# Performance work log

Measured on AMD Instinct MI355X. Metric: run time of the kernel, lower is better.

## Reference

```python
import jax, jax.numpy as jnp
import numpy as np

# Config (mirrors init_kwargs)
B, S = 1, 2048          # batch, seq_len
H = 2048                # hidden_size
NH, NKV = 16, 8         # attention heads, kv heads (GQA n_rep = 2)
HD = H // NH            # head_dim = 128
I = 5632                # intermediate_size
L = 2                   # num_hidden_layers
V = 32000               # vocab_size
WIN = 1024              # sliding_window
THETA = 10000.0
EPS = 1e-6


def setup_inputs() -> dict:
    key = jax.random.key(0)
    ks = jax.random.split(key, 12)
    s = 0.02
    return {
        "input_ids": jax.random.randint(ks[0], (B, S), 0, V, dtype=jnp.int32),
        "embed": jax.random.normal(ks[1], (V, H), jnp.float32) * s,
        "Wq": jax.random.normal(ks[2], (L, H, NH * HD), jnp.float32) * s,
        "Wk": jax.random.normal(ks[3], (L, H, NKV * HD), jnp.float32) * s,
        "Wv": jax.random.normal(ks[4], (L, H, NKV * HD), jnp.float32) * s,
        "Wo": jax.random.normal(ks[5], (L, NH * HD, H), jnp.float32) * s,
        "Wg": jax.random.normal(ks[6], (L, H, I), jnp.float32) * s,
        "Wu": jax.random.normal(ks[7], (L, H, I), jnp.float32) * s,
        "Wd": jax.random.normal(ks[8], (L, I, H), jnp.float32) * s,
        "ln1": jnp.ones((L, H), jnp.float32),
        "ln2": jnp.ones((L, H), jnp.float32),
        "norm_w": jnp.ones((H,), jnp.float32),
    }


def _rmsnorm(x, w, eps=EPS):
    return x * jax.lax.rsqrt(jnp.mean(x * x, axis=-1, keepdims=True) + eps) * w


def _rope_tables(seq_len, dim, theta):
    inv_freq = 1.0 / (theta ** (jnp.arange(0, dim, 2, dtype=jnp.float32) / dim))
    freqs = jnp.arange(seq_len, dtype=jnp.float32)[:, None] * inv_freq[None, :]  # [S, dim/2]
    emb = jnp.concatenate([freqs, freqs], axis=-1)  # [S, dim]
    return jnp.cos(emb), jnp.sin(emb)


def _rotate_half(x):
    half = x.shape[-1] // 2
    return jnp.concatenate([-x[..., half:], x[..., :half]], axis=-1)


def _sliding_window_causal_mask(seq_len, window, dtype):
    i = jnp.arange(seq_len)[:, None]
    j = jnp.arange(seq_len)[None, :]
    allowed = (j <= i) & (j >= i - window)  # band: causal + sliding window
    return jnp.where(allowed, 0.0, jnp.finfo(dtype).min).astype(dtype)[None, None]  # [1,1,S,S]


def _forward(input_ids, embed, Wq, Wk, Wv, Wo, Wg, Wu, Wd, ln1, ln2, norm_w):
    x = embed[input_ids]  # [B,S,H]
    cos, sin = _rope_tables(S, HD, THETA)          # [S,HD]
    cos = cos[None, :, None, :]                    # [1,S,1,HD]
    sin = sin[None, :, None, :]
    mask = _sliding_window_causal_mask(S, WIN, x.dtype)  # [1,1,S,S]
    scale = 1.0 / jnp.sqrt(jnp.float32(HD)).astype(x.dtype)
    n_rep = NH // NKV

    for l in range(L):
        # --- attention block ---
        h = _rmsnorm(x, ln1[l])
        q = (h @ Wq[l]).reshape(B, S, NH, HD)
        k = (h @ Wk[l]).reshape(B, S, NKV, HD)
        v = (h @ Wv[l]).reshape(B, S, NKV, HD)
        q = q * cos + _rotate_half(q) * sin
        k = k * cos + _rotate_half(k) * sin
        # repeat_kv (GQA)
        k = jnp.broadcast_to(k[:, :, :, None, :], (B, S, NKV, n_rep, HD)).reshape(B, S, NH, HD)
        v = jnp.broadcast_to(v[:, :, :, None, :], (B, S, NKV, n_rep, HD)).reshape(B, S, NH, HD)
        scores = jnp.einsum('bshn,bthn->bhst', q, k) * scale + mask  # [B,NH,S,S]
        attn = jax.nn.softmax(scores.astype(jnp.float32), axis=-1).astype(x.dtype)
        o = jnp.einsum('bhst,bthn->bshn', attn, v).reshape(B, S, NH * HD)
        x = x + o @ Wo[l]
        # --- MLP block (SwiGLU) ---
        h = _rmsnorm(x, ln2[l])
        x = x + (jax.nn.silu(h @ Wg[l]) * (h @ Wu[l])) @ Wd[l]

    return _rmsnorm(x, norm_w)


def reference(input_ids, embed, Wq, Wk, Wv, Wo, Wg, Wu, Wd, ln1, ln2, norm_w):
    return _forward(input_ids, embed, Wq, Wk, Wv, Wo, Wg, Wu, Wd, ln1, ln2, norm_w)
```

## Files before the change

kernel.cpp:

```cpp
#include <hip/hip_runtime.h>
#include <stdint.h>

using bf16x8 = __attribute__((ext_vector_type(8))) __bf16;
using f32x4  = __attribute__((ext_vector_type(4))) float;

#define DEVI __device__ __forceinline__

DEVI unsigned short f2b(float f) {
  unsigned int u = __builtin_bit_cast(unsigned int, f);
  u = (u + 0x7FFFu + ((u >> 16) & 1u)) >> 16;
  return (unsigned short)u;
}
DEVI float b2f(unsigned short h) {
  unsigned int u = ((unsigned int)h) << 16;
  return __builtin_bit_cast(float, u);
}
DEVI f32x4 mfma16(bf16x8 a, bf16x8 b, f32x4 c) {
  return __builtin_amdgcn_mfma_f32_16x16x32_bf16(a, b, c, 0, 0, 0);
}
#define GLD(gp, lp) __builtin_amdgcn_global_load_lds( \
    (__attribute__((address_space(1))) void*)(uintptr_t)(gp), \
    (__attribute__((address_space(3))) void*)(uintptr_t)(lp), 16, 0, 0)

static constexpr int S_LEN = 2048;
static constexpr int HDIM  = 2048;
static constexpr int NH    = 16;
static constexpr int NKV   = 8;
static constexpr int HD    = 128;
static constexpr int IFF   = 5632;
static constexpr int WIN   = 1024;

__global__ __launch_bounds__(64) void rope_tables_kernel(float* __restrict__ ct,
                                                         float* __restrict__ st) {
  int s = blockIdx.x, d = threadIdx.x;
  float inv = expf(-(float)d * (9.210340371976184f / 64.0f));
  float f = (float)s * inv;
  ct[s * 64 + d] = cosf(f);
  st[s * 64 + d] = sinf(f);
}

__global__ __launch_bounds__(256) void gather_kernel(const int* __restrict__ ids,
    const float* __restrict__ embed, float* __restrict__ x) {
  int s = blockIdx.x, t = threadIdx.x;
  const float4* src = (const float4*)(embed + (size_t)ids[s] * HDIM);
  float4* dst = (float4*)(x + (size_t)s * HDIM);
  dst[t]       = src[t];
  dst[t + 256] = src[t + 256];
}

DEVI void rms_finish(float4 v0, float4 v1, const float* __restrict__ w,
                     void* __restrict__ outp, int s, int t, int outf32) {
  float ss = v0.x*v0.x + v0.y*v0.y + v0.z*v0.z + v0.w*v0.w +
             v1.x*v1.x + v1.y*v1.y + v1.z*v1.z + v1.w*v1.w;
  #pragma unroll
  for (int off = 32; off >= 1; off >>= 1) ss += __shfl_xor(ss, off, 64);
  __shared__ float red[4];
  if ((t & 63) == 0) red[t >> 6] = ss;
  __syncthreads();
  ss = red[0] + red[1] + red[2] + red[3];
  float rr = rsqrtf(ss * (1.0f / 2048.0f) + 1e-6f);
  const float4* w4 = (const float4*)w;
  float4 w0 = w4[t], w1 = w4[t + 256];
  float o0x = v0.x*rr*w0.x, o0y = v0.y*rr*w0.y, o0z = v0.z*rr*w0.z, o0w = v0.w*rr*w0.w;
  float o1x = v1.x*rr*w1.x, o1y = v1.y*rr*w1.y, o1z = v1.z*rr*w1.z, o1w = v1.w*rr*w1.w;
  if (outf32) {
    float4* o4 = (float4*)outp + (size_t)s * 512;
    o4[t]       = make_float4(o0x, o0y, o0z, o0w);
    o4[t + 256] = make_float4(o1x, o1y, o1z, o1w);
  } else {
    uint2* ob = (uint2*)((unsigned short*)outp + (size_t)s * HDIM);
    ob[t]       = make_uint2((unsigned)f2b(o0x) | ((unsigned)f2b(o0y) << 16),
                             (unsigned)f2b(o0z) | ((unsigned)f2b(o0w) << 16));
    ob[t + 256] = make_uint2((unsigned)f2b(o1x) | ((unsigned)f2b(o1y) << 16),
                             (unsigned)f2b(o1z) | ((unsigned)f2b(o1w) << 16));
  }
}

__global__ __launch_bounds__(256) void rmsnorm_kernel(const float* __restrict__ x,
    const float* __restrict__ w, void* __restrict__ outp) {
  int s = blockIdx.x, t = threadIdx.x;
  const float4* row = (const float4*)(x + (size_t)s * HDIM);
  rms_finish(row[t], row[t + 256], w, outp, s, t, 0);
}

template<int OUTF32>
__global__ __launch_bounds__(256) void rmsnorm_combine_kernel(
    float* __restrict__ x, const float* __restrict__ parts,
    const float* __restrict__ w, void* __restrict__ outp) {
  int s = blockIdx.x, t = threadIdx.x;
  const size_t PS = (size_t)2048 * 2048;
  float4* row = (float4*)(x + (size_t)s * HDIM);
  float4 v0 = row[t], v1 = row[t + 256];
  #pragma unroll
  for (int p = 0; p < 4; ++p) {
    const float4* pr = (const float4*)(parts + p * PS + (size_t)s * HDIM);
    float4 a = pr[t], b = pr[t + 256];
    v0.x += a.x; v0.y += a.y; v0.z += a.z; v0.w += a.w;
    v1.x += b.x; v1.y += b.y; v1.z += b.z; v1.w += b.w;
  }
  row[t] = v0; row[t + 256] = v1;
  rms_finish(v0, v1, w, outp, s, t, OUTF32);
}

__global__ __launch_bounds__(256) void rope_apply_kernel(const float* __restrict__ qkv,
    const float* __restrict__ qkv2,
    const float* __restrict__ ct, const float* __restrict__ st,
    unsigned short* __restrict__ qo, unsigned short* __restrict__ ko) {
  int s = blockIdx.x, t = threadIdx.x;
  #pragma unroll
  for (int it = 0; it < 6; ++it) {
    int idx = it * 256 + t;
    int head = idx >> 6, d = idx & 63;
    float c = ct[s * 64 + d], sn = st[s * 64 + d];
    if (head < NH) {
      const float* base  = qkv  + (size_t)s * 4096 + head * HD;
      const float* base2 = qkv2 + (size_t)s * 4096 + head * HD;
      float a = base[d] + base2[d], b = base[d + 64] + base2[d + 64];
      unsigned short* dst = qo + (size_t)s * (NH * HD) + head * HD;
      dst[d]      = f2b(a * c - b * sn);
      dst[d + 64] = f2b(b * c + a * sn);
    } else {
      int kh = head - NH;
      const float* base  = qkv  + (size_t)s * 4096 + 2048 + kh * HD;
      const float* base2 = qkv2 + (size_t)s * 4096 + 2048 + kh * HD;
      float a = base[d] + base2[d], b = base[d + 64] + base2[d + 64];
      unsigned short* dst = ko + (size_t)s * (NKV * HD) + kh * HD;
      dst[d]      = f2b(a * c - b * sn);
      dst[d + 64] = f2b(b * c + a * sn);
    }
  }
}

DEVI void tile_transpose_cvt(const float* __restrict__ in, int istr,
    unsigned short* __restrict__ out, int ostr, int k0, int n0, int ob, float* tl) {
  int tx = threadIdx.x & 63, ty = threadIdx.x >> 6;
  #pragma unroll
  for (int i = 0; i < 16; ++i)
    tl[(ty + 4 * i) * 65 + tx] = in[(size_t)(k0 + ty + 4 * i) * istr + (n0 + tx)];
  __syncthreads();
  #pragma unroll
  for (int i = 0; i < 16; ++i)
    out[(size_t)(ob + ty + 4 * i) * ostr + (k0 + tx)] = f2b(tl[tx * 65 + (ty + 4 * i)]);
}

__global__ __launch_bounds__(256) void convert_weights_kernel(
    const float* __restrict__ Wq, const float* __restrict__ Wk,
    const float* __restrict__ Wv, const float* __restrict__ Wo,
    const float* __restrict__ Wg, const float* __restrict__ Wu,
    const float* __restrict__ Wd,
    unsigned short* wqkvT, unsigned short* woT,
    unsigned short* wguT, unsigned short* wdT) {
  __shared__ float tl[64 * 65];
  int b = blockIdx.x;
  const float* in; unsigned short* out; int istr, ostr, tilesN, t; int guAdd = -1;
  if (b < 1024)      { in = Wq; out = wqkvT;                       istr = 2048; ostr = 2048; tilesN = 32; t = b; }
  else if (b < 1536) { in = Wk; out = wqkvT + (size_t)2048 * 2048; istr = 1024; ostr = 2048; tilesN = 16; t = b - 1024; }
  else if (b < 2048) { in = Wv; out = wqkvT + (size_t)3072 * 2048; istr = 1024; ostr = 2048; tilesN = 16; t = b - 1536; }
  else if (b < 3072) { in = Wo; out = woT;                         istr = 2048; ostr = 2048; tilesN = 32; t = b - 2048; }
  else if (b < 5888) { in = Wg; out = wguT;                        istr = 5632; ostr = 2048; tilesN = 88; t = b - 3072; guAdd = 0; }
  else if (b < 8704) { in = Wu; out = wguT;                        istr = 5632; ostr = 2048; tilesN = 88; t = b - 5888; guAdd = 128; }
  else               { in = Wd; out = wdT;                         istr = 2048; ostr = 5632; tilesN = 32; t = b - 8704; }
  int k0 = (t / tilesN) * 64, n0 = (t % tilesN) * 64;
  int ob = (guAdd >= 0) ? (((n0 >> 7) << 8) + (n0 & 64) + guAdd) : n0;
  tile_transpose_cvt(in, istr, out, ostr, k0, n0, ob, tl);
}

__global__ __launch_bounds__(256) void transpose_cvt_sum_kernel(
    const float* __restrict__ in, const float* __restrict__ in2, int istr,
    unsigned short* __restrict__ out, int ostr, int tilesN) {
  __shared__ float tl[64 * 65];
  int t = blockIdx.x;
  int k0 = (t / tilesN) * 64, n0 = (t % tilesN) * 64;
  int tx = threadIdx.x & 63, ty = threadIdx.x >> 6;
  #pragma unroll
  for (int i = 0; i < 16; ++i) {
    size_t idx = (size_t)(k0 + ty + 4 * i) * istr + (n0 + tx);
    tl[(ty + 4 * i) * 65 + tx] = in[idx] + in2[idx];
  }
  __syncthreads();
  #pragma unroll
  for (int i = 0; i < 16; ++i)
    out[(size_t)(n0 + ty + 4 * i) * ostr + (k0 + tx)] = f2b(tl[tx * 65 + (ty + 4 * i)]);
}

DEVI bf16x8 ldsAB(const unsigned short* buf, int r, int cbyte) {
  return *(const bf16x8*)((const unsigned char*)buf + r * 128 + (cbyte ^ ((r & 7) << 4)));
}
DEVI void stage_unit(const unsigned short* __restrict__ G, int Kstr,
                     unsigned short* lbuf, int loff0, int grow0,
                     int loff1, int grow1, int w, int l) {
  const int rsub = l >> 3;
  const int ce = ((l & 7) ^ rsub) << 3;
  const unsigned short* s0 = G + (size_t)(grow0 + w * 8 + rsub) * Kstr + ce;
  GLD(s0, (unsigned char*)lbuf + loff0 + w * 1024 + l * 16);
  const unsigned short* s1 = G + (size_t)(grow1 + w * 8 + rsub) * Kstr + ce;
  GLD(s1, (unsigned char*)lbuf + loff1 + w * 1024 + l * 16);
}
template<int Q>
DEVI void phase_mfma(const unsigned short* Ab, f32x4 (&acc)[8][4],
                     bf16x8 (&breg)[2][4], int wr, int lg, int li) {
  const int r0 = wr * 128 + Q * 32 + li;
  bf16x8 a00 = ldsAB(Ab, r0,      lg * 16);
  bf16x8 a01 = ldsAB(Ab, r0 + 16, lg * 16);
  bf16x8 a10 = ldsAB(Ab, r0,      64 + lg * 16);
  bf16x8 a11 = ldsAB(Ab, r0 + 16, 64 + lg * 16);
  __builtin_amdgcn_s_setprio(1);
  #pragma unroll
  for (int n = 0; n < 4; ++n) {
    acc[Q*2][n]   = mfma16(a00, breg[0][n], acc[Q*2][n]);
    acc[Q*2+1][n] = mfma16(a01, breg[0][n], acc[Q*2+1][n]);
  }
  #pragma unroll
  for (int n = 0; n < 4; ++n) {
    acc[Q*2][n]   = mfma16(a10, breg[1][n], acc[Q*2][n]);
    acc[Q*2+1][n] = mfma16(a11, breg[1][n], acc[Q*2+1][n]);
  }
  __builtin_amdgcn_s_setprio(0);
}

template<int EPI>
__global__ __launch_bounds__(512, 2) void gemm256_kernel(
    const unsigned short* __restrict__ A, const unsigned short* __restrict__ Bt,
    void* __restrict__ Cout, int Kstr, int nt, int parts, int nbx, int ldc,
    long long partStride) {
  __shared__ __align__(16) unsigned char smem[131072];
  unsigned short* As0 = (unsigned short*)smem;
  unsigned short* Bs0 = (unsigned short*)(smem + 65536);
  const int tid = threadIdx.x, l = tid & 63, w = tid >> 6;
  const int lg = l >> 4, li = l & 15;
  const int wr = w >> 2, wc = w & 3;
  const int nb = gridDim.x, qx = nb >> 3;
  const int wg = ((int)blockIdx.x & 7) * qx + ((int)blockIdx.x >> 3);
  const int nbT = nb / parts;
  const int tile = wg % nbT, part = wg / nbT;
  const int m0 = (tile / nbx) * 256, n0 = (tile % nbx) * 256;
  const int kOff = part * (nt << 6);
  const unsigned short* At  = A  + (size_t)m0 * Kstr + kOff;
  const unsigned short* Bto = Bt + (size_t)n0 * Kstr + kOff;
  f32x4 acc[8][4] = {};
  bf16x8 breg[2][4];

  stage_unit(At,  Kstr, As0, 0, 0, 16384, 128, w, l);
  stage_unit(Bto, Kstr, Bs0, 0, 0, 8192,  64,  w, l);
  stage_unit(Bto, Kstr, Bs0, 16384, 128, 24576, 192, w, l);
  stage_unit(At,  Kstr, As0, 8192, 64, 24576, 192, w, l);
  { int k1 = (nt > 1) ? 64 : 0;
    stage_unit(At + k1, Kstr, As0 + 16384, 0, 0, 16384, 128, w, l); }
  asm volatile("s_waitcnt vmcnt(4)\n\ts_barrier" ::: "memory");

  for (int t = 0; t < nt; ++t) {
    unsigned short* Ab  = As0 + (t & 1) * 16384;
    unsigned short* Bb  = Bs0 + (t & 1) * 16384;
    unsigned short* Abn = As0 + ((t & 1) ^ 1) * 16384;
    unsigned short* Bbn = Bs0 + ((t & 1) ^ 1) * 16384;
    const int kt1 = ((t + 1 < nt) ? t + 1 : nt - 1) << 6;
    const int kt2 = ((t + 2 < nt) ? t + 2 : nt - 1) << 6;
    stage_unit(Bto + kt1, Kstr, Bbn, 0, 0, 8192, 64, w, l);
    #pragma unroll
    for (int ks = 0; ks < 2; ++ks)
      #pragma unroll
      for (int n = 0; n < 4; ++n)
        breg[ks][n] = ldsAB(Bb, wc * 64 + n * 16 + li, ks * 64 + lg * 16);
    phase_mfma<0>(Ab, acc, breg, wr, lg, li);
    stage_unit(Bto + kt1, Kstr, Bbn, 16384, 128, 24576, 192, w, l);
    phase_mfma<1>(Ab, acc, breg, wr, lg, li);
    asm volatile("s_waitcnt vmcnt(6)\n\ts_barrier" ::: "memory");
    stage_unit(At + kt1, Kstr, Abn, 8192, 64, 24576, 192, w, l);
    phase_mfma<2>(Ab, acc, breg, wr, lg, li);
    stage_unit(At + kt2, Kstr, Ab, 0, 0, 16384, 128, w, l);
    phase_mfma<3>(Ab, acc, breg, wr, lg, li);
    asm volatile("s_waitcnt vmcnt(4)\n\ts_barrier" ::: "memory");
  }
  asm volatile("s_waitcnt vmcnt(0)" ::: "memory");

  if (EPI == 0) {
    float* C = (float*)Cout + (size_t)part * (size_t)partStride;
    #pragma unroll
    for (int m = 0; m < 8; ++m)
      #pragma unroll
      for (int n = 0; n < 4; ++n) {
        int col = n0 + wc * 64 + n * 16 + li;
        #pragma unroll
        for (int r = 0; r < 4; ++r) {
          int row = m0 + wr * 128 + m * 16 + lg * 4 + r;
          C[(size_t)row * ldc + col] = acc[m][n][r];
        }
      }
  } else {
    float* ub = (float*)smem;
    asm volatile("s_barrier" ::: "memory");
    if (wc >= 2) {
      #pragma unroll
      for (int m = 0; m < 8; ++m)
        #pragma unroll
        for (int n = 0; n < 4; ++n) {
          int colL = (wc - 2) * 64 + n * 16 + li;
          #pragma unroll
          for (int r = 0; r < 4; ++r) {
            int rowl = wr * 128 + m * 16 + lg * 4 + r;
            ub[rowl * 128 + colL] = acc[m][n][r];
          }
        }
    }
    asm volatile("s_barrier" ::: "memory");
    if (wc < 2) {
      unsigned short* act = (unsigned short*)Cout;
      const int col0 = n0 >> 1;
      #pragma unroll
      for (int m = 0; m < 8; ++m)
        #pragma unroll
        for (int n = 0; n < 4; ++n) {
          int colL = wc * 64 + n * 16 + li;
          #pragma unroll
          for (int r = 0; r < 4; ++r) {
            int rowl = wr * 128 + m * 16 + lg * 4 + r;
            float g = acc[m][n][r];
            float u = ub[rowl * 128 + colL];
            act[(size_t)(m0 + rowl) * ldc + col0 + colL] =
                f2b(g / (1.0f + __expf(-g)) * u);
          }
        }
    }
  }
}

__global__ __launch_bounds__(256) void attn_kernel(
    const unsigned short* __restrict__ qg, const unsigned short* __restrict__ kg,
    const unsigned short* __restrict__ vtg, unsigned short* __restrict__ og) {
  __shared__ __align__(16) unsigned short Klds[64 * 128];
  __shared__ __align__(16) unsigned short Vtlds[128 * 64];
  __shared__ __align__(16) unsigned short Plds[4][16 * 72];
  const int tid = threadIdx.x, l = tid & 63, w = tid >> 6;
  const int lg = l >> 4, li = l & 15;
  const int i0 = blockIdx.x * 64, hq = blockIdx.y;
  const int kv = hq >> 1;
  const int qr0 = i0 + w * 16;
  const float scale = 0.08838834764831845f;

  bf16x8 qf[4];
  {
    const unsigned short* qrow = qg + (size_t)(qr0 + li) * (NH * HD) + hq * HD;
    #pragma unroll
    for (int sl = 0; sl < 4; ++sl)
      qf[sl] = *(const bf16x8*)(qrow + sl * 32 + lg * 8);
  }
  f32x4 oacc[8] = {};
  float mrow[4] = {-1e30f, -1e30f, -1e30f, -1e30f};
  float srow[4] = {0.f, 0.f, 0.f, 0.f};

  int jstart = i0 - WIN; if (jstart < 0) jstart = 0;
  for (int j0 = jstart; j0 <= i0; j0 += 64) {
    #pragma unroll
    for (int p = 0; p < 4; ++p) {
      int off = p * 4096 + w * 1024 + l * 16;
      int row = off >> 8;
      int colb = (off & 255) ^ ((row & 7) << 4);
      const unsigned short* ga = kg + (size_t)(j0 + row) * (NKV * HD) + kv * HD + (colb >> 1);
      GLD(ga, &Klds[(p * 4096 + w * 1024) >> 1]);
    }
    #pragma unroll
    for (int p = 0; p < 4; ++p) {
      int off = p * 4096 + w * 1024 + l * 16;
      int d = off >> 7;
      int colb = (off & 127) ^ ((d & 7) << 4);
      const unsigned short* ga = vtg + (size_t)(kv * HD + d) * S_LEN + j0 + (colb >> 1);
      GLD(ga, &Vtlds[(p * 4096 + w * 1024) >> 1]);
    }
    __syncthreads();

    f32x4 sacc[4] = {};
    #pragma unroll
    for (int nt = 0; nt < 4; ++nt) {
      int kr = nt * 16 + li;
      #pragma unroll
      for (int sl = 0; sl < 4; ++sl) {
        int cb = (sl * 64 + lg * 16) ^ ((kr & 7) << 4);
        bf16x8 kf = *(const bf16x8*)&Klds[(kr * 256 + cb) >> 1];
        sacc[nt] = mfma16(qf[sl], kf, sacc[nt]);
      }
    }

    float pv[4][4];
    #pragma unroll
    for (int r = 0; r < 4; ++r) {
      int qi = qr0 + lg * 4 + r;
      float sval[4];
      float tm = -1e30f;
      #pragma unroll
      for (int nt = 0; nt < 4; ++nt) {
        int j = j0 + nt * 16 + li;
        bool ok = (j <= qi) && (j + WIN >= qi);
        float sv = ok ? sacc[nt][r] * scale : -1e30f;
        sval[nt] = sv;
        tm = fmaxf(tm, sv);
      }
      #pragma unroll
      for (int off2 = 1; off2 < 16; off2 <<= 1)
        tm = fmaxf(tm, __shfl_xor(tm, off2, 64));
      float mnew = fmaxf(mrow[r], tm);
      float resc = __expf(mrow[r] - mnew);
      mrow[r] = mnew;
      float rs = 0.f;
      #pragma unroll
      for (int nt = 0; nt < 4; ++nt) {
        float p = (sval[nt] > -9e29f) ? __expf(sval[nt] - mnew) : 0.f;
        pv[nt][r] = p;
        rs += p;
      }
      #pragma unroll
      for (int off2 = 1; off2 < 16; off2 <<= 1)
        rs += __shfl_xor(rs, off2, 64);
      srow[r] = srow[r] * resc + rs;
      #pragma unroll
      for (int dt = 0; dt < 8; ++dt) oacc[dt][r] *= resc;
    }

    #pragma unroll
    for (int r = 0; r < 4; ++r)
      #pragma unroll
      for (int nt = 0; nt < 4; ++nt)
        Plds[w][(lg * 4 + r) * 72 + nt * 16 + li] = f2b(pv[nt][r]);
    bf16x8 ap[2];
    #pragma unroll
    for (int ks = 0; ks < 2; ++ks)
      ap[ks] = *(const bf16x8*)&Plds[w][li * 72 + ks * 32 + lg * 8];
    #pragma unroll
    for (int dt = 0; dt < 8; ++dt) {
      int d = dt * 16 + li;
      #pragma unroll
      for (int ks = 0; ks < 2; ++ks) {
        int cb = (ks * 64 + lg * 16) ^ ((d & 7) << 4);
        bf16x8 vf = *(const bf16x8*)&Vtlds[(d * 128 + cb) >> 1];
        oacc[dt] = mfma16(ap[ks], vf, oacc[dt]);
      }
    }
    __syncthreads();
  }

  #pragma unroll
  for (int r = 0; r < 4; ++r) {
    float inv = 1.0f / srow[r];
    int qi = qr0 + lg * 4 + r;
    unsigned short* orow = og + (size_t)qi * (NH * HD) + hq * HD;
    #pragma unroll
    for (int dt = 0; dt < 8; ++dt)
      orow[dt * 16 + li] = f2b(oacc[dt][r] * inv);
  }
}

extern "C" void kernel_launch(void* const* d_in, const int* in_sizes, int n_in,
                              void* d_out, int out_size, void* d_ws, size_t ws_size,
                              hipStream_t stream) {
  const int*   ids   = (const int*)d_in[0];
  const float* embed = (const float*)d_in[1];
  const float* Wq    = (const float*)d_in[2];
  const float* Wk    = (const float*)d_in[3];
  const float* Wv    = (const float*)d_in[4];
  const float* Wo    = (const float*)d_in[5];
  const float* Wg    = (const float*)d_in[6];
  const float* Wu    = (const float*)d_in[7];
  const float* Wd    = (const float*)d_in[8];
  const float* ln1   = (const float*)d_in[9];
  const float* ln2   = (const float*)d_in[10];
  const float* normw = (const float*)d_in[11];

  uint8_t* ws = (uint8_t*)d_ws;
  unsigned short* wqkvT = (unsigned short*)(ws + 0);
  unsigned short* woT   = (unsigned short*)(ws + 16777216ull);
  unsigned short* wguT  = (unsigned short*)(ws + 25165824ull);
  unsigned short* wdT   = (unsigned short*)(ws + 71303168ull);
  float*          x     = (float*)(ws + 94371840ull);
  unsigned short* h     = (unsigned short*)(ws + 111149056ull);
  unsigned short* q     = (unsigned short*)(ws + 119537664ull);
  unsigned short* k     = (unsigned short*)(ws + 127926272ull);
  unsigned short* vt    = (unsigned short*)(ws + 132120576ull);
  unsigned short* o     = (unsigned short*)(ws + 136314880ull);
  unsigned short* act   = (unsigned short*)(ws + 119537664ull);
  float*          pbuf  = (float*)(ws + 144703488ull);
  float*          cost  = (float*)(ws + 213909504ull);
  float*          sint  = (float*)(ws + 214433792ull);
  const long long PSq = 8388608LL;
  const long long PSo = 4194304LL;

  rope_tables_kernel<<<2048, 64, 0, stream>>>(cost, sint);
  gather_kernel<<<2048, 256, 0, stream>>>(ids, embed, x);

  for (int l = 0; l < 2; ++l) {
    convert_weights_kernel<<<11520, 256, 0, stream>>>(
        Wq + (size_t)l * 2048 * 2048, Wk + (size_t)l * 2048 * 1024,
        Wv + (size_t)l * 2048 * 1024, Wo + (size_t)l * 2048 * 2048,
        Wg + (size_t)l * 2048 * 5632, Wu + (size_t)l * 2048 * 5632,
        Wd + (size_t)l * 5632 * 2048,
        wqkvT, woT, wguT, wdT);
    if (l == 0)
      rmsnorm_kernel<<<2048, 256, 0, stream>>>(x, ln1, h);
    else
      rmsnorm_combine_kernel<0><<<2048, 256, 0, stream>>>(x, pbuf, ln1 + 2048, h);
    gemm256_kernel<0><<<256, 512, 0, stream>>>(h, wqkvT, pbuf, 2048, 16, 2, 16, 4096, PSq);
    rope_apply_kernel<<<2048, 256, 0, stream>>>(pbuf, pbuf + PSq, cost, sint, q, k);
    transpose_cvt_sum_kernel<<<512, 256, 0, stream>>>(pbuf + 3072, pbuf + PSq + 3072, 4096, vt, 2048, 16);
    attn_kernel<<<dim3(32, 16), 256, 0, stream>>>(q, k, vt, o);
    gemm256_kernel<0><<<256, 512, 0, stream>>>(o, woT, pbuf, 2048, 8, 4, 8, 2048, PSo);
    rmsnorm_combine_kernel<0><<<2048, 256, 0, stream>>>(x, pbuf, ln2 + l * 2048, h);
    gemm256_kernel<3><<<352, 512, 0, stream>>>(h, wguT, act, 2048, 32, 1, 44, 5632, 0);
    gemm256_kernel<0><<<256, 512, 0, stream>>>(act, wdT, pbuf, 5632, 22, 4, 8, 2048, PSo);
  }
  rmsnorm_combine_kernel<1><<<2048, 256, 0, stream>>>(x, pbuf, normw, d_out);
  (void)in_sizes; (void)n_in; (void)out_size; (void)ws_size;
}
```

Before: 778.0 us.

## Switch GEMMs to 128x256 tiles, double-buffer attention KV, fuse small kernels

GEMMs move from 256x256 to 128x256 output tiles with a reworked LDS staging schedule, and use fewer split-K parts: the QKV GEMM is no longer split, the others use two parts instead of four. The rmsnorm-combine kernel now sums only two partials. Attention processes both GQA query heads sharing a KV head in one 512-thread block, with double-buffered K/V tile loads. The RoPE table build is fused into the gather kernel, and RoPE application plus the V transpose are merged into one kernel. The intent is less partial-sum traffic, more reuse of KV loads, and fewer launches, at the cost of lower per-tile arithmetic intensity in the GEMMs and more LDS per attention block.

```diff
diff --git a/kernel.cpp b/kernel.cpp
--- a/kernel.cpp
+++ b/kernel.cpp
@@ -30,22 +30,20 @@
 static constexpr int IFF   = 5632;
 static constexpr int WIN   = 1024;
 
-__global__ __launch_bounds__(64) void rope_tables_kernel(float* __restrict__ ct,
-                                                         float* __restrict__ st) {
-  int s = blockIdx.x, d = threadIdx.x;
-  float inv = expf(-(float)d * (9.210340371976184f / 64.0f));
-  float f = (float)s * inv;
-  ct[s * 64 + d] = cosf(f);
-  st[s * 64 + d] = sinf(f);
-}
-
 __global__ __launch_bounds__(256) void gather_kernel(const int* __restrict__ ids,
-    const float* __restrict__ embed, float* __restrict__ x) {
+    const float* __restrict__ embed, float* __restrict__ x,
+    float* __restrict__ ct, float* __restrict__ st) {
   int s = blockIdx.x, t = threadIdx.x;
   const float4* src = (const float4*)(embed + (size_t)ids[s] * HDIM);
   float4* dst = (float4*)(x + (size_t)s * HDIM);
   dst[t]       = src[t];
   dst[t + 256] = src[t + 256];
+  if (t < 64) {
+    float inv = expf(-(float)t * (9.210340371976184f / 64.0f));
+    float f = (float)s * inv;
+    ct[s * 64 + t] = cosf(f);
+    st[s * 64 + t] = sinf(f);
+  }
 }
 
 DEVI void rms_finish(float4 v0, float4 v1, const float* __restrict__ w,
@@ -83,7 +81,7 @@
   rms_finish(row[t], row[t + 256], w, outp, s, t, 0);
 }
 
-template<int OUTF32>
+template<int OUTF32, int NPARTS>
 __global__ __launch_bounds__(256) void rmsnorm_combine_kernel(
     float* __restrict__ x, const float* __restrict__ parts,
     const float* __restrict__ w, void* __restrict__ outp) {
@@ -92,7 +90,7 @@
   float4* row = (float4*)(x + (size_t)s * HDIM);
   float4 v0 = row[t], v1 = row[t + 256];
   #pragma unroll
-  for (int p = 0; p < 4; ++p) {
+  for (int p = 0; p < NPARTS; ++p) {
     const float4* pr = (const float4*)(parts + p * PS + (size_t)s * HDIM);
     float4 a = pr[t], b = pr[t + 256];
     v0.x += a.x; v0.y += a.y; v0.z += a.z; v0.w += a.w;
@@ -102,32 +100,46 @@
   rms_finish(v0, v1, w, outp, s, t, OUTF32);
 }
 
-__global__ __launch_bounds__(256) void rope_apply_kernel(const float* __restrict__ qkv,
-    const float* __restrict__ qkv2,
+__global__ __launch_bounds__(256) void posttrans_kernel(const float* __restrict__ qkvf,
     const float* __restrict__ ct, const float* __restrict__ st,
-    unsigned short* __restrict__ qo, unsigned short* __restrict__ ko) {
-  int s = blockIdx.x, t = threadIdx.x;
-  #pragma unroll
-  for (int it = 0; it < 6; ++it) {
-    int idx = it * 256 + t;
-    int head = idx >> 6, d = idx & 63;
-    float c = ct[s * 64 + d], sn = st[s * 64 + d];
-    if (head < NH) {
-      const float* base  = qkv  + (size_t)s * 4096 + head * HD;
-      const float* base2 = qkv2 + (size_t)s * 4096 + head * HD;
-      float a = base[d] + base2[d], b = base[d + 64] + base2[d + 64];
-      unsigned short* dst = qo + (size_t)s * (NH * HD) + head * HD;
-      dst[d]      = f2b(a * c - b * sn);
-      dst[d + 64] = f2b(b * c + a * sn);
-    } else {
-      int kh = head - NH;
-      const float* base  = qkv  + (size_t)s * 4096 + 2048 + kh * HD;
-      const float* base2 = qkv2 + (size_t)s * 4096 + 2048 + kh * HD;
-      float a = base[d] + base2[d], b = base[d + 64] + base2[d + 64];
-      unsigned short* dst = ko + (size_t)s * (NKV * HD) + kh * HD;
-      dst[d]      = f2b(a * c - b * sn);
-      dst[d + 64] = f2b(b * c + a * sn);
+    unsigned short* __restrict__ qo, unsigned short* __restrict__ ko,
+    unsigned short* __restrict__ vt) {
+  __shared__ float tl[64 * 65];
+  int b = blockIdx.x;
+  if (b < 2048) {
+    int s = b, t = threadIdx.x;
+    #pragma unroll
+    for (int it = 0; it < 6; ++it) {
+      int idx = it * 256 + t;
+      int head = idx >> 6, d = idx & 63;
+      float c = ct[s * 64 + d], sn = st[s * 64 + d];
+      if (head < NH) {
+        const float* base = qkvf + (size_t)s * 4096 + head * HD;
+        float a = base[d], bb = base[d + 64];
+        unsigned short* dst = qo + (size_t)s * (NH * HD) + head * HD;
+        dst[d]      = f2b(a * c - bb * sn);
+        dst[d + 64] = f2b(bb * c + a * sn);
+      } else {
+        int kh = head - NH;
+        const float* base = qkvf + (size_t)s * 4096 + 2048 + kh * HD;
+        float a = base[d], bb = base[d + 64];
+        unsigned short* dst = ko + (size_t)s * (NKV * HD) + kh * HD;
+        dst[d]      = f2b(a * c - bb * sn);
+        dst[d + 64] = f2b(bb * c + a * sn);
+      }
     }
+  } else {
+    int t = b - 2048;
+    int k0 = (t / 16) * 64, n0 = (t % 16) * 64;
+    int tx = threadIdx.x & 63, ty = threadIdx.x >> 6;
+    const float* in = qkvf + 3072;
+    #pragma unroll
+    for (int i = 0; i < 16; ++i)
+      tl[(ty + 4 * i) * 65 + tx] = in[(size_t)(k0 + ty + 4 * i) * 4096 + (n0 + tx)];
+    __syncthreads();
+    #pragma unroll
+    for (int i = 0; i < 16; ++i)
+      vt[(size_t)(n0 + ty + 4 * i) * 2048 + (k0 + tx)] = f2b(tl[tx * 65 + (ty + 4 * i)]);
   }
 }
 
@@ -165,24 +177,6 @@
   tile_transpose_cvt(in, istr, out, ostr, k0, n0, ob, tl);
 }
 
-__global__ __launch_bounds__(256) void transpose_cvt_sum_kernel(
-    const float* __restrict__ in, const float* __restrict__ in2, int istr,
-    unsigned short* __restrict__ out, int ostr, int tilesN) {
-  __shared__ float tl[64 * 65];
-  int t = blockIdx.x;
-  int k0 = (t / tilesN) * 64, n0 = (t % tilesN) * 64;
-  int tx = threadIdx.x & 63, ty = threadIdx.x >> 6;
-  #pragma unroll
-  for (int i = 0; i < 16; ++i) {
-    size_t idx = (size_t)(k0 + ty + 4 * i) * istr + (n0 + tx);
-    tl[(ty + 4 * i) * 65 + tx] = in[idx] + in2[idx];
-  }
-  __syncthreads();
-  #pragma unroll
-  for (int i = 0; i < 16; ++i)
-    out[(size_t)(n0 + ty + 4 * i) * ostr + (k0 + tx)] = f2b(tl[tx * 65 + (ty + 4 * i)]);
-}
-
 DEVI bf16x8 ldsAB(const unsigned short* buf, int r, int cbyte) {
   return *(const bf16x8*)((const unsigned char*)buf + r * 128 + (cbyte ^ ((r & 7) << 4)));
 }
@@ -197,35 +191,27 @@
   GLD(s1, (unsigned char*)lbuf + loff1 + w * 1024 + l * 16);
 }
 template<int Q>
-DEVI void phase_mfma(const unsigned short* Ab, f32x4 (&acc)[8][4],
-                     bf16x8 (&breg)[2][4], int wr, int lg, int li) {
-  const int r0 = wr * 128 + Q * 32 + li;
-  bf16x8 a00 = ldsAB(Ab, r0,      lg * 16);
-  bf16x8 a01 = ldsAB(Ab, r0 + 16, lg * 16);
-  bf16x8 a10 = ldsAB(Ab, r0,      64 + lg * 16);
-  bf16x8 a11 = ldsAB(Ab, r0 + 16, 64 + lg * 16);
+DEVI void phase128(const unsigned short* Ab, f32x4 (&acc)[4][4],
+                   bf16x8 (&breg)[2][4], int wr, int lg, int li) {
+  const int r0 = wr * 64 + Q * 16 + li;
+  bf16x8 a0 = ldsAB(Ab, r0, lg * 16);
+  bf16x8 a1 = ldsAB(Ab, r0, 64 + lg * 16);
   __builtin_amdgcn_s_setprio(1);
   #pragma unroll
-  for (int n = 0; n < 4; ++n) {
-    acc[Q*2][n]   = mfma16(a00, breg[0][n], acc[Q*2][n]);
-    acc[Q*2+1][n] = mfma16(a01, breg[0][n], acc[Q*2+1][n]);
-  }
-  #pragma unroll
-  for (int n = 0; n < 4; ++n) {
-    acc[Q*2][n]   = mfma16(a10, breg[1][n], acc[Q*2][n]);
-    acc[Q*2+1][n] = mfma16(a11, breg[1][n], acc[Q*2+1][n]);
-  }
+  for (int n = 0; n < 4; ++n) acc[Q][n] = mfma16(a0, breg[0][n], acc[Q][n]);
+  #pragma unroll
+  for (int n = 0; n < 4; ++n) acc[Q][n] = mfma16(a1, breg[1][n], acc[Q][n]);
   __builtin_amdgcn_s_setprio(0);
 }
 
 template<int EPI>
-__global__ __launch_bounds__(512, 2) void gemm256_kernel(
+__global__ __launch_bounds__(512, 1) void gemm128_kernel(
     const unsigned short* __restrict__ A, const unsigned short* __restrict__ Bt,
-    void* __restrict__ Cout, int Kstr, int nt, int parts, int nbx, int ldc,
+    void* __restrict__ Cout, int Kstr, int nt, int parts, int nbm, int ldc,
     long long partStride) {
-  __shared__ __align__(16) unsigned char smem[131072];
+  __shared__ __align__(16) unsigned char smem[98304];
   unsigned short* As0 = (unsigned short*)smem;
-  unsigned short* Bs0 = (unsigned short*)(smem + 65536);
+  unsigned short* Bs0 = (unsigned short*)(smem + 32768);
   const int tid = threadIdx.x, l = tid & 63, w = tid >> 6;
   const int lg = l >> 4, li = l & 15;
   const int wr = w >> 2, wc = w & 3;
@@ -233,56 +219,54 @@
   const int wg = ((int)blockIdx.x & 7) * qx + ((int)blockIdx.x >> 3);
   const int nbT = nb / parts;
   const int tile = wg % nbT, part = wg / nbT;
-  const int m0 = (tile / nbx) * 256, n0 = (tile % nbx) * 256;
+  const int m0 = (tile % nbm) * 128, n0 = (tile / nbm) * 256;
   const int kOff = part * (nt << 6);
   const unsigned short* At  = A  + (size_t)m0 * Kstr + kOff;
   const unsigned short* Bto = Bt + (size_t)n0 * Kstr + kOff;
-  f32x4 acc[8][4] = {};
+  f32x4 acc[4][4] = {};
   bf16x8 breg[2][4];
 
-  stage_unit(At,  Kstr, As0, 0, 0, 16384, 128, w, l);
-  stage_unit(Bto, Kstr, Bs0, 0, 0, 8192,  64,  w, l);
+  stage_unit(Bto, Kstr, Bs0, 0, 0, 8192, 64, w, l);
   stage_unit(Bto, Kstr, Bs0, 16384, 128, 24576, 192, w, l);
-  stage_unit(At,  Kstr, As0, 8192, 64, 24576, 192, w, l);
+  stage_unit(At,  Kstr, As0, 0, 0, 8192, 64, w, l);
   { int k1 = (nt > 1) ? 64 : 0;
-    stage_unit(At + k1, Kstr, As0 + 16384, 0, 0, 16384, 128, w, l); }
+    stage_unit(Bto + k1, Kstr, Bs0 + 16384, 0, 0, 8192, 64, w, l);
+    stage_unit(Bto + k1, Kstr, Bs0 + 16384, 16384, 128, 24576, 192, w, l); }
   asm volatile("s_waitcnt vmcnt(4)\n\ts_barrier" ::: "memory");
 
   for (int t = 0; t < nt; ++t) {
-    unsigned short* Ab  = As0 + (t & 1) * 16384;
+    unsigned short* Ab  = As0 + (t & 1) * 8192;
     unsigned short* Bb  = Bs0 + (t & 1) * 16384;
-    unsigned short* Abn = As0 + ((t & 1) ^ 1) * 16384;
-    unsigned short* Bbn = Bs0 + ((t & 1) ^ 1) * 16384;
+    unsigned short* Abn = As0 + ((t & 1) ^ 1) * 8192;
     const int kt1 = ((t + 1 < nt) ? t + 1 : nt - 1) << 6;
     const int kt2 = ((t + 2 < nt) ? t + 2 : nt - 1) << 6;
-    stage_unit(Bto + kt1, Kstr, Bbn, 0, 0, 8192, 64, w, l);
+    stage_unit(At + kt1, Kstr, Abn, 0, 0, 8192, 64, w, l);
     #pragma unroll
     for (int ks = 0; ks < 2; ++ks)
       #pragma unroll
       for (int n = 0; n < 4; ++n)
         breg[ks][n] = ldsAB(Bb, wc * 64 + n * 16 + li, ks * 64 + lg * 16);
-    phase_mfma<0>(Ab, acc, breg, wr, lg, li);
-    stage_unit(Bto + kt1, Kstr, Bbn, 16384, 128, 24576, 192, w, l);
-    phase_mfma<1>(Ab, acc, breg, wr, lg, li);
-    asm volatile("s_waitcnt vmcnt(6)\n\ts_barrier" ::: "memory");
-    stage_unit(At + kt1, Kstr, Abn, 8192, 64, 24576, 192, w, l);
-    phase_mfma<2>(Ab, acc, breg, wr, lg, li);
-    stage_unit(At + kt2, Kstr, Ab, 0, 0, 16384, 128, w, l);
-    phase_mfma<3>(Ab, acc, breg, wr, lg, li);
-    asm volatile("s_waitcnt vmcnt(4)\n\ts_barrier" ::: "memory");
+    asm volatile("s_waitcnt lgkmcnt(0)\n\ts_barrier" ::: "memory");
+    phase128<0>(Ab, acc, breg, wr, lg, li);
+    stage_unit(Bto + kt2, Kstr, Bb, 0, 0, 8192, 64, w, l);
+    phase128<1>(Ab, acc, breg, wr, lg, li);
+    stage_unit(Bto + kt2, Kstr, Bb, 16384, 128, 24576, 192, w, l);
+    phase128<2>(Ab, acc, breg, wr, lg, li);
+    phase128<3>(Ab, acc, breg, wr, lg, li);
+    asm volatile("s_waitcnt vmcnt(4) lgkmcnt(0)\n\ts_barrier" ::: "memory");
   }
   asm volatile("s_waitcnt vmcnt(0)" ::: "memory");
 
   if (EPI == 0) {
     float* C = (float*)Cout + (size_t)part * (size_t)partStride;
     #pragma unroll
-    for (int m = 0; m < 8; ++m)
+    for (int m = 0; m < 4; ++m)
       #pragma unroll
       for (int n = 0; n < 4; ++n) {
         int col = n0 + wc * 64 + n * 16 + li;
         #pragma unroll
         for (int r = 0; r < 4; ++r) {
-          int row = m0 + wr * 128 + m * 16 + lg * 4 + r;
+          int row = m0 + wr * 64 + m * 16 + lg * 4 + r;
           C[(size_t)row * ldc + col] = acc[m][n][r];
         }
       }
@@ -291,29 +275,29 @@
     asm volatile("s_barrier" ::: "memory");
     if (wc >= 2) {
       #pragma unroll
-      for (int m = 0; m < 8; ++m)
+      for (int m = 0; m < 4; ++m)
         #pragma unroll
         for (int n = 0; n < 4; ++n) {
           int colL = (wc - 2) * 64 + n * 16 + li;
           #pragma unroll
           for (int r = 0; r < 4; ++r) {
-            int rowl = wr * 128 + m * 16 + lg * 4 + r;
+            int rowl = wr * 64 + m * 16 + lg * 4 + r;
             ub[rowl * 128 + colL] = acc[m][n][r];
           }
         }
     }
-    asm volatile("s_barrier" ::: "memory");
+    asm volatile("s_waitcnt lgkmcnt(0)\n\ts_barrier" ::: "memory");
     if (wc < 2) {
       unsigned short* act = (unsigned short*)Cout;
       const int col0 = n0 >> 1;
       #pragma unroll
-      for (int m = 0; m < 8; ++m)
+      for (int m = 0; m < 4; ++m)
         #pragma unroll
         for (int n = 0; n < 4; ++n) {
           int colL = wc * 64 + n * 16 + li;
           #pragma unroll
           for (int r = 0; r < 4; ++r) {
-            int rowl = wr * 128 + m * 16 + lg * 4 + r;
+            int rowl = wr * 64 + m * 16 + lg * 4 + r;
             float g = acc[m][n][r];
             float u = ub[rowl * 128 + colL];
             act[(size_t)(m0 + rowl) * ldc + col0 + colL] =
@@ -324,17 +308,38 @@
   }
 }
 
-__global__ __launch_bounds__(256) void attn_kernel(
+DEVI void stageKV(const unsigned short* __restrict__ kg,
+                  const unsigned short* __restrict__ vtg, int kv, int j0,
+                  unsigned short* Kbuf, unsigned short* Vbuf, int w, int l) {
+  #pragma unroll
+  for (int p = 0; p < 2; ++p) {
+    int off = p * 8192 + w * 1024 + l * 16;
+    int row = off >> 8;
+    int colb = (off & 255) ^ ((row & 7) << 4);
+    GLD(kg + (size_t)(j0 + row) * (NKV * HD) + kv * HD + (colb >> 1),
+        (unsigned char*)Kbuf + off);
+  }
+  #pragma unroll
+  for (int p = 0; p < 2; ++p) {
+    int off = p * 8192 + w * 1024 + l * 16;
+    int d = off >> 7;
+    int colb = (off & 127) ^ ((d & 7) << 4);
+    GLD(vtg + (size_t)(kv * HD + d) * S_LEN + j0 + (colb >> 1),
+        (unsigned char*)Vbuf + off);
+  }
+}
+
+__global__ __launch_bounds__(512) void attn_kernel(
     const unsigned short* __restrict__ qg, const unsigned short* __restrict__ kg,
     const unsigned short* __restrict__ vtg, unsigned short* __restrict__ og) {
-  __shared__ __align__(16) unsigned short Klds[64 * 128];
-  __shared__ __align__(16) unsigned short Vtlds[128 * 64];
-  __shared__ __align__(16) unsigned short Plds[4][16 * 72];
+  __shared__ __align__(16) unsigned short Kl[2][64 * 128];
+  __shared__ __align__(16) unsigned short Vtl[2][128 * 64];
+  __shared__ __align__(16) unsigned short Plds[8][16 * 72];
   const int tid = threadIdx.x, l = tid & 63, w = tid >> 6;
   const int lg = l >> 4, li = l & 15;
-  const int i0 = blockIdx.x * 64, hq = blockIdx.y;
-  const int kv = hq >> 1;
-  const int qr0 = i0 + w * 16;
+  const int i0 = blockIdx.x * 64, kv = blockIdx.y;
+  const int hq = kv * 2 + (w >> 2);
+  const int qr0 = i0 + (w & 3) * 16;
   const float scale = 0.08838834764831845f;
 
   bf16x8 qf[4];
@@ -349,24 +354,16 @@
   float srow[4] = {0.f, 0.f, 0.f, 0.f};
 
   int jstart = i0 - WIN; if (jstart < 0) jstart = 0;
-  for (int j0 = jstart; j0 <= i0; j0 += 64) {
-    #pragma unroll
-    for (int p = 0; p < 4; ++p) {
-      int off = p * 4096 + w * 1024 + l * 16;
-      int row = off >> 8;
-      int colb = (off & 255) ^ ((row & 7) << 4);
-      const unsigned short* ga = kg + (size_t)(j0 + row) * (NKV * HD) + kv * HD + (colb >> 1);
-      GLD(ga, &Klds[(p * 4096 + w * 1024) >> 1]);
-    }
-    #pragma unroll
-    for (int p = 0; p < 4; ++p) {
-      int off = p * 4096 + w * 1024 + l * 16;
-      int d = off >> 7;
-      int colb = (off & 127) ^ ((d & 7) << 4);
-      const unsigned short* ga = vtg + (size_t)(kv * HD + d) * S_LEN + j0 + (colb >> 1);
-      GLD(ga, &Vtlds[(p * 4096 + w * 1024) >> 1]);
-    }
-    __syncthreads();
+  stageKV(kg, vtg, kv, jstart, Kl[0], Vtl[0], w, l);
+
+  int it = 0;
+  for (int j0 = jstart; j0 <= i0; j0 += 64, ++it) {
+    const int cur = it & 1;
+    asm volatile("s_waitcnt vmcnt(0) lgkmcnt(0)\n\ts_barrier" ::: "memory");
+    if (j0 + 64 <= i0)
+      stageKV(kg, vtg, kv, j0 + 64, Kl[cur ^ 1], Vtl[cur ^ 1], w, l);
+    const unsigned short* Klds  = Kl[cur];
+    const unsigned short* Vtlds = Vtl[cur];
 
     f32x4 sacc[4] = {};
     #pragma unroll
@@ -434,7 +431,6 @@
         oacc[dt] = mfma16(ap[ks], vf, oacc[dt]);
       }
     }
-    __syncthreads();
   }
 
   #pragma unroll
@@ -479,11 +475,9 @@
   float*          pbuf  = (float*)(ws + 144703488ull);
   float*          cost  = (float*)(ws + 213909504ull);
   float*          sint  = (float*)(ws + 214433792ull);
-  const long long PSq = 8388608LL;
   const long long PSo = 4194304LL;
 
-  rope_tables_kernel<<<2048, 64, 0, stream>>>(cost, sint);
-  gather_kernel<<<2048, 256, 0, stream>>>(ids, embed, x);
+  gather_kernel<<<2048, 256, 0, stream>>>(ids, embed, x, cost, sint);
 
   for (int l = 0; l < 2; ++l) {
     convert_weights_kernel<<<11520, 256, 0, stream>>>(
@@ -495,16 +489,15 @@
     if (l == 0)
       rmsnorm_kernel<<<2048, 256, 0, stream>>>(x, ln1, h);
     else
-      rmsnorm_combine_kernel<0><<<2048, 256, 0, stream>>>(x, pbuf, ln1 + 2048, h);
-    gemm256_kernel<0><<<256, 512, 0, stream>>>(h, wqkvT, pbuf, 2048, 16, 2, 16, 4096, PSq);
-    rope_apply_kernel<<<2048, 256, 0, stream>>>(pbuf, pbuf + PSq, cost, sint, q, k);
-    transpose_cvt_sum_kernel<<<512, 256, 0, stream>>>(pbuf + 3072, pbuf + PSq + 3072, 4096, vt, 2048, 16);
-    attn_kernel<<<dim3(32, 16), 256, 0, stream>>>(q, k, vt, o);
-    gemm256_kernel<0><<<256, 512, 0, stream>>>(o, woT, pbuf, 2048, 8, 4, 8, 2048, PSo);
-    rmsnorm_combine_kernel<0><<<2048, 256, 0, stream>>>(x, pbuf, ln2 + l * 2048, h);
-    gemm256_kernel<3><<<352, 512, 0, stream>>>(h, wguT, act, 2048, 32, 1, 44, 5632, 0);
-    gemm256_kernel<0><<<256, 512, 0, stream>>>(act, wdT, pbuf, 5632, 22, 4, 8, 2048, PSo);
-  }
-  rmsnorm_combine_kernel<1><<<2048, 256, 0, stream>>>(x, pbuf, normw, d_out);
+      rmsnorm_combine_kernel<0, 2><<<2048, 256, 0, stream>>>(x, pbuf, ln1 + 2048, h);
+    gemm128_kernel<0><<<256, 512, 0, stream>>>(h, wqkvT, pbuf, 2048, 32, 1, 16, 4096, 0);
+    posttrans_kernel<<<2560, 256, 0, stream>>>(pbuf, cost, sint, q, k, vt);
+    attn_kernel<<<dim3(32, 8), 512, 0, stream>>>(q, k, vt, o);
+    gemm128_kernel<0><<<256, 512, 0, stream>>>(o, woT, pbuf, 2048, 16, 2, 16, 2048, PSo);
+    rmsnorm_combine_kernel<0, 2><<<2048, 256, 0, stream>>>(x, pbuf, ln2 + l * 2048, h);
+    gemm128_kernel<3><<<704, 512, 0, stream>>>(h, wguT, act, 2048, 32, 1, 16, 5632, 0);
+    gemm128_kernel<0><<<256, 512, 0, stream>>>(act, wdT, pbuf, 5632, 44, 2, 16, 2048, PSo);
+  }
+  rmsnorm_combine_kernel<1, 2><<<2048, 256, 0, stream>>>(x, pbuf, normw, d_out);
   (void)in_sizes; (void)n_in; (void)out_size; (void)ws_size;
 }
```

After: 699.0 us. 10.2% less time.
